# Optimization experiments

Measured on AMD Instinct MI355X. Metric: run time of the kernel, lower is better.

The kernel has to match this reference:

```python
import jax, jax.numpy as jnp
import numpy as np

LN_EPS = 1e-5

def _layernorm(x, gamma, beta):
    mu = jnp.mean(x, axis=-1, keepdims=True)
    var = jnp.mean((x - mu) ** 2, axis=-1, keepdims=True)
    return (x - mu) * jax.lax.rsqrt(var + LN_EPS) * gamma + beta

def setup_inputs() -> dict:
    key = jax.random.key(0)
    ks = jax.random.split(key, 12)
    n_drug, n_dis, E = 10000, 10000, 1000000
    feat = 128          # in_units * 2
    d_in = 2 * feat     # in_units * 4 = 256
    hid = 128
    hid2 = hid // 2
    def lin(kw, kb, fan_in, fan_out):
        bound = 1.0 / np.sqrt(fan_in)
        W = jax.random.uniform(kw, (fan_in, fan_out), jnp.float32, -bound, bound)
        b = jax.random.uniform(kb, (fan_out,), jnp.float32, -bound, bound)
        return W, b
    W1, b1 = lin(ks[0], ks[1], d_in, hid)
    W2, b2 = lin(ks[2], ks[3], hid, hid2)
    W3, b3 = lin(ks[4], ks[5], hid2, 1)
    return {
        "drug_feat": jax.random.normal(ks[6], (n_drug, feat), jnp.float32),
        "dis_feat": jax.random.normal(ks[7], (n_dis, feat), jnp.float32),
        "src_idx": jax.random.randint(ks[8], (E,), 0, n_drug, jnp.int32),
        "dst_idx": jax.random.randint(ks[9], (E,), 0, n_dis, jnp.int32),
        "W1": W1, "b1": b1,
        "g1": jnp.ones((hid,), jnp.float32), "be1": jnp.zeros((hid,), jnp.float32),
        "W2": W2, "b2": b2,
        "g2": jnp.ones((hid2,), jnp.float32), "be2": jnp.zeros((hid2,), jnp.float32),
        "W3": W3, "b3": b3,
    }

def reference(drug_feat, dis_feat, src_idx, dst_idx,
              W1, b1, g1, be1, W2, b2, g2, be2, W3, b3):
    # apply_edges: gather src (drug) and dst (disease) features, concat -> [E, 4*in_units]
    m = jnp.concatenate([drug_feat[src_idx], dis_feat[dst_idx]], axis=1)
    h = jax.nn.gelu(_layernorm(m @ W1 + b1, g1, be1), approximate=False)
    h = jax.nn.gelu(_layernorm(h @ W2 + b2, g2, be2), approximate=False)
    return h @ W3 + b3  # [E, 1]
```

## Files before the change

### kernel.cpp

```cpp
#include <hip/hip_runtime.h>
#include <hip/hip_bf16.h>

typedef __attribute__((ext_vector_type(4))) float f32x4;
typedef __attribute__((ext_vector_type(8))) short bf16x8;

#define MFMA16(a, b, c) __builtin_amdgcn_mfma_f32_16x16x32_bf16((a), (b), (c), 0, 0, 0)

#define W1T_OFF 0
#define B1_OFF  65536
#define G1_OFF  66048
#define E1_OFF  66560
#define B2_OFF  67072
#define G2_OFF  67328
#define E2_OFF  67584
#define W3_OFF  67840
#define B3_OFF  68096
#define SMEM_BYTES 68128

__device__ __forceinline__ short f2bf(float x) {
  __hip_bfloat16 h = __float2bfloat16(x);
  return __builtin_bit_cast(short, h);
}

__device__ __forceinline__ bf16x8 pack8(f32x4 a, f32x4 b) {
  bf16x8 r;
  r[0] = f2bf(a[0]); r[1] = f2bf(a[1]); r[2] = f2bf(a[2]); r[3] = f2bf(a[3]);
  r[4] = f2bf(b[0]); r[5] = f2bf(b[1]); r[6] = f2bf(b[2]); r[7] = f2bf(b[3]);
  return r;
}

__device__ __forceinline__ float gelu_fast(float z) {
  float s = z * z;
  float y = z * __builtin_fmaf(-0.10180479f, s, -2.3048496f);
  float t = __builtin_amdgcn_exp2f(y);
  return z * __builtin_amdgcn_rcpf(1.0f + t);
}

__global__ __launch_bounds__(256) void prep_weights(
    const float* __restrict__ W1, const float* __restrict__ W2,
    short* __restrict__ w1i, short* __restrict__ w2L) {
  int idx = blockIdx.x * 256 + threadIdx.x;
  if (idx < 32768) {
    int k = idx >> 7, n = idx & 127;
    w1i[n * 256 + ((((k >> 3) ^ (n & 7)) << 3) | (k & 7))] = f2bf(W1[idx]);
  } else if (idx < 40960) {
    int j = idx - 32768;
    int n = j >> 6, n2 = j & 63;
    int kb2 = n >> 5;
    int qf = (n >> 2) & 3;
    int e = ((n >> 4) & 1) * 4 + (n & 3);
    int t = n2 >> 4, cc2 = n2 & 15;
    w2L[(kb2 * 4 + t) * 512 + (qf * 16 + cc2) * 8 + e] = f2bf(W2[j]);
  }
}

__global__ __launch_bounds__(256) void prep_feats(
    const float* __restrict__ f, short* __restrict__ o, int n8) {
  int idx = blockIdx.x * 256 + threadIdx.x;
  if (idx < n8) {
    f32x4 a = *(const f32x4*)(f + idx * 8);
    f32x4 b = *(const f32x4*)(f + idx * 8 + 4);
    *(bf16x8*)(o + idx * 8) = pack8(a, b);
  }
}

__global__ __launch_bounds__(1024) __attribute__((amdgpu_waves_per_eu(2)))
void mlp_fused(
    const short* __restrict__ drugb, const short* __restrict__ disb,
    const int* __restrict__ src, const int* __restrict__ dst,
    const short* __restrict__ w1i, const short* __restrict__ w2L,
    const float* __restrict__ b1, const float* __restrict__ g1, const float* __restrict__ be1,
    const float* __restrict__ b2, const float* __restrict__ g2, const float* __restrict__ be2,
    const float* __restrict__ W3, const float* __restrict__ b3,
    float* __restrict__ out, int E, int ntiles) {
  extern __shared__ char smem[];
  short* w1t = (short*)(smem + W1T_OFF);
  float* b1s = (float*)(smem + B1_OFF);
  float* g1s = (float*)(smem + G1_OFF);
  float* e1s = (float*)(smem + E1_OFF);
  float* b2s = (float*)(smem + B2_OFF);
  float* g2s = (float*)(smem + G2_OFF);
  float* e2s = (float*)(smem + E2_OFF);
  float* w3s = (float*)(smem + W3_OFF);
  float* b3s = (float*)(smem + B3_OFF);

  const int tid  = threadIdx.x;
  const int wave = tid >> 6;
  const int lane = tid & 63;
  const int q    = lane >> 4;
  const int cc   = lane & 15;

  #pragma unroll
  for (int o = 0; o < 4; ++o) {
    int s = (tid + o * 1024) * 8;
    *(bf16x8*)(w1t + s) = *(const bf16x8*)(w1i + s);
  }
  if (tid < 128) { b1s[tid] = b1[tid]; g1s[tid] = g1[tid]; e1s[tid] = be1[tid]; }
  else if (tid < 192) { int j = tid - 128; b2s[j] = b2[j]; g2s[j] = g2[j]; e2s[j] = be2[j]; w3s[j] = W3[j]; }
  if (tid == 256) b3s[0] = b3[0];
  __syncthreads();

  const short* w2p = w2L + (lane << 3);

  for (int tile = blockIdx.x; tile < ntiles; tile += gridDim.x) {
    const int r  = tile * 256 + wave * 16 + cc;
    const int rc = (r < E) ? r : (E - 1);
    const short* pd = drugb + (size_t)src[rc] * 128 + q * 8;
    const short* pq = disb  + (size_t)dst[rc] * 128 + q * 8;

    f32x4 acc1[8];
    #pragma unroll
    for (int nt = 0; nt < 8; ++nt)
      acc1[nt] = *(const f32x4*)(b1s + nt * 16 + q * 4);

    bf16x8 u = *(const bf16x8*)pd;
    #pragma unroll 1
    for (int kb = 0; kb < 8; ++kb) {
      bf16x8 bfr = u;
      if (kb < 7) {
        const short* pn = (kb < 3) ? (pd + (kb + 1) * 32) : (pq + (kb - 3) * 32);
        u = *(const bf16x8*)pn;
      }
      const char* abase = (const char*)w1t + cc * 512 + ((((kb * 4 + q) ^ (cc & 7))) << 4);
      #pragma unroll
      for (int nt = 0; nt < 8; ++nt) {
        bf16x8 af = *(const bf16x8*)(abase + nt * 8192);
        acc1[nt] = MFMA16(af, bfr, acc1[nt]);
      }
    }

    bf16x8 hreg[4];
    {
      float s = 0.f, ss = 0.f;
      #pragma unroll
      for (int nt = 0; nt < 8; ++nt)
        #pragma unroll
        for (int j = 0; j < 4; ++j) { float v = acc1[nt][j]; s += v; ss += v * v; }
      s  += __shfl_xor(s, 16);  s  += __shfl_xor(s, 32);
      ss += __shfl_xor(ss, 16); ss += __shfl_xor(ss, 32);
      float mu   = s * 0.0078125f;
      float var  = ss * 0.0078125f - mu * mu;
      var = (var > 0.f) ? var : 0.f;
      float rstd = __builtin_amdgcn_rsqf(var + 1e-5f);

      #pragma unroll
      for (int h = 0; h < 4; ++h) {
        f32x4 glo = *(const f32x4*)(g1s + (2 * h) * 16 + q * 4);
        f32x4 elo = *(const f32x4*)(e1s + (2 * h) * 16 + q * 4);
        f32x4 ghi = *(const f32x4*)(g1s + (2 * h + 1) * 16 + q * 4);
        f32x4 ehi = *(const f32x4*)(e1s + (2 * h + 1) * 16 + q * 4);
        f32x4 a, b;
        #pragma unroll
        for (int j = 0; j < 4; ++j) {
          a[j] = gelu_fast(__builtin_fmaf((acc1[2 * h][j] - mu) * rstd, glo[j], elo[j]));
          b[j] = gelu_fast(__builtin_fmaf((acc1[2 * h + 1][j] - mu) * rstd, ghi[j], ehi[j]));
        }
        hreg[h] = pack8(a, b);
      }
    }

    f32x4 acc2[4];
    #pragma unroll
    for (int t = 0; t < 4; ++t)
      acc2[t] = *(const f32x4*)(b2s + t * 16 + q * 4);

    #pragma unroll
    for (int kb2 = 0; kb2 < 4; ++kb2) {
      bf16x8 hb = hreg[kb2];
      #pragma unroll
      for (int t = 0; t < 4; ++t) {
        bf16x8 af = *(const bf16x8*)(w2p + (kb2 * 4 + t) * 512);
        acc2[t] = MFMA16(af, hb, acc2[t]);
      }
      __builtin_amdgcn_sched_barrier(0);
    }

    {
      float s = 0.f, ss = 0.f;
      #pragma unroll
      for (int t = 0; t < 4; ++t)
        #pragma unroll
        for (int j = 0; j < 4; ++j) { float v = acc2[t][j]; s += v; ss += v * v; }
      s  += __shfl_xor(s, 16);  s  += __shfl_xor(s, 32);
      ss += __shfl_xor(ss, 16); ss += __shfl_xor(ss, 32);
      float mu   = s * 0.015625f;
      float var  = ss * 0.015625f - mu * mu;
      var = (var > 0.f) ? var : 0.f;
      float rstd = __builtin_amdgcn_rsqf(var + 1e-5f);

      float dot = 0.f;
      #pragma unroll
      for (int t = 0; t < 4; ++t) {
        f32x4 gv = *(const f32x4*)(g2s + t * 16 + q * 4);
        f32x4 ev = *(const f32x4*)(e2s + t * 16 + q * 4);
        f32x4 wv = *(const f32x4*)(w3s + t * 16 + q * 4);
        #pragma unroll
        for (int j = 0; j < 4; ++j) {
          float zz = __builtin_fmaf((acc2[t][j] - mu) * rstd, gv[j], ev[j]);
          dot = __builtin_fmaf(gelu_fast(zz), wv[j], dot);
        }
      }
      dot += __shfl_xor(dot, 16); dot += __shfl_xor(dot, 32);
      if (q == 0 && r < E) out[r] = dot + b3s[0];
    }
  }
}

extern "C" void kernel_launch(void* const* d_in, const int* in_sizes, int n_in,
                              void* d_out, int out_size, void* d_ws, size_t ws_size,
                              hipStream_t stream) {
  const float* drug = (const float*)d_in[0];
  const float* dis  = (const float*)d_in[1];
  const int*   src  = (const int*)d_in[2];
  const int*   dst  = (const int*)d_in[3];
  const float* W1   = (const float*)d_in[4];
  const float* b1   = (const float*)d_in[5];
  const float* g1   = (const float*)d_in[6];
  const float* be1  = (const float*)d_in[7];
  const float* W2   = (const float*)d_in[8];
  const float* b2   = (const float*)d_in[9];
  const float* g2   = (const float*)d_in[10];
  const float* be2  = (const float*)d_in[11];
  const float* W3   = (const float*)d_in[12];
  const float* b3   = (const float*)d_in[13];
  float* out = (float*)d_out;

  const int E      = in_sizes[2];
  const int ndrug8 = in_sizes[0] / 8;
  const int ndis8  = in_sizes[1] / 8;
  const int ntiles = (E + 255) / 256;

  short* w1i   = (short*)d_ws;
  short* w2L   = w1i + 32768;
  short* drugb = w2L + 8192;
  short* disb  = drugb + (size_t)ndrug8 * 8;

  (void)hipFuncSetAttribute((const void*)mlp_fused,
                            hipFuncAttributeMaxDynamicSharedMemorySize, SMEM_BYTES);

  prep_weights<<<dim3(160), dim3(256), 0, stream>>>(W1, W2, w1i, w2L);
  prep_feats<<<dim3((ndrug8 + 255) / 256), dim3(256), 0, stream>>>(drug, drugb, ndrug8);
  prep_feats<<<dim3((ndis8 + 255) / 256), dim3(256), 0, stream>>>(dis, disb, ndis8);

  int grid = 512;
  if (ntiles < grid) grid = ntiles;
  mlp_fused<<<dim3(grid), dim3(1024), SMEM_BYTES, stream>>>(
      drugb, disb, src, dst, w1i, w2L,
      b1, g1, be1, b2, g2, be2, W3, b3, out, E, ntiles);
}
```

Before: 247.5 us.

## Process two 16-row edge groups per wave to reuse W1/W2 LDS fragments

Each wave now handles 32 edges (two 16-row MFMA column blocks) instead of 16, so every W1 and W2 fragment read from LDS feeds two MFMAs. The block shrinks to 512 threads with launch bounds of 2 blocks per CU, keeping 256 edges per tile. This halves LDS traffic per edge and gives more independent MFMAs to hide latency. The cost is roughly double the accumulator registers per wave, which lowers occupancy and means fewer in-flight waves for gather latency.

```diff
diff --git a/kernel.cpp b/kernel.cpp
--- a/kernel.cpp
+++ b/kernel.cpp
@@ -64,8 +64,7 @@
   }
 }
 
-__global__ __launch_bounds__(1024) __attribute__((amdgpu_waves_per_eu(2)))
-void mlp_fused(
+__global__ __launch_bounds__(512, 2) void mlp_fused(
     const short* __restrict__ drugb, const short* __restrict__ disb,
     const int* __restrict__ src, const int* __restrict__ dst,
     const short* __restrict__ w1i, const short* __restrict__ w2L,
@@ -91,8 +90,8 @@
   const int cc   = lane & 15;
 
   #pragma unroll
-  for (int o = 0; o < 4; ++o) {
-    int s = (tid + o * 1024) * 8;
+  for (int o = 0; o < 8; ++o) {
+    int s = (tid + o * 512) * 8;
     *(bf16x8*)(w1t + s) = *(const bf16x8*)(w1i + s);
   }
   if (tid < 128) { b1s[tid] = b1[tid]; g1s[tid] = g1[tid]; e1s[tid] = be1[tid]; }
@@ -103,45 +102,63 @@
   const short* w2p = w2L + (lane << 3);
 
   for (int tile = blockIdx.x; tile < ntiles; tile += gridDim.x) {
-    const int r  = tile * 256 + wave * 16 + cc;
-    const int rc = (r < E) ? r : (E - 1);
-    const short* pd = drugb + (size_t)src[rc] * 128 + q * 8;
-    const short* pq = disb  + (size_t)dst[rc] * 128 + q * 8;
-
-    f32x4 acc1[8];
+    const int r0  = tile * 256 + wave * 32 + cc;
+    const int rc0 = (r0 < E) ? r0 : (E - 1);
+    const int rc1 = (r0 + 16 < E) ? (r0 + 16) : (E - 1);
+    const short* pd0 = drugb + (size_t)src[rc0] * 128 + q * 8;
+    const short* pq0 = disb  + (size_t)dst[rc0] * 128 + q * 8;
+    const short* pd1 = drugb + (size_t)src[rc1] * 128 + q * 8;
+    const short* pq1 = disb  + (size_t)dst[rc1] * 128 + q * 8;
+
+    f32x4 acc1[8][2];
     #pragma unroll
-    for (int nt = 0; nt < 8; ++nt)
-      acc1[nt] = *(const f32x4*)(b1s + nt * 16 + q * 4);
-
-    bf16x8 u = *(const bf16x8*)pd;
+    for (int nt = 0; nt < 8; ++nt) {
+      f32x4 bv = *(const f32x4*)(b1s + nt * 16 + q * 4);
+      acc1[nt][0] = bv;
+      acc1[nt][1] = bv;
+    }
+
+    bf16x8 u0 = *(const bf16x8*)pd0;
+    bf16x8 u1 = *(const bf16x8*)pd1;
     #pragma unroll 1
     for (int kb = 0; kb < 8; ++kb) {
-      bf16x8 bfr = u;
+      bf16x8 f0 = u0, f1 = u1;
       if (kb < 7) {
-        const short* pn = (kb < 3) ? (pd + (kb + 1) * 32) : (pq + (kb - 3) * 32);
-        u = *(const bf16x8*)pn;
+        const short* pn0 = (kb < 3) ? (pd0 + (kb + 1) * 32) : (pq0 + (kb - 3) * 32);
+        const short* pn1 = (kb < 3) ? (pd1 + (kb + 1) * 32) : (pq1 + (kb - 3) * 32);
+        u0 = *(const bf16x8*)pn0;
+        u1 = *(const bf16x8*)pn1;
       }
       const char* abase = (const char*)w1t + cc * 512 + ((((kb * 4 + q) ^ (cc & 7))) << 4);
       #pragma unroll
       for (int nt = 0; nt < 8; ++nt) {
         bf16x8 af = *(const bf16x8*)(abase + nt * 8192);
-        acc1[nt] = MFMA16(af, bfr, acc1[nt]);
-      }
-    }
-
-    bf16x8 hreg[4];
+        acc1[nt][0] = MFMA16(af, f0, acc1[nt][0]);
+        acc1[nt][1] = MFMA16(af, f1, acc1[nt][1]);
+      }
+    }
+
+    bf16x8 hreg[4][2];
     {
-      float s = 0.f, ss = 0.f;
+      float s0 = 0.f, ss0 = 0.f, s1 = 0.f, ss1 = 0.f;
       #pragma unroll
       for (int nt = 0; nt < 8; ++nt)
         #pragma unroll
-        for (int j = 0; j < 4; ++j) { float v = acc1[nt][j]; s += v; ss += v * v; }
-      s  += __shfl_xor(s, 16);  s  += __shfl_xor(s, 32);
-      ss += __shfl_xor(ss, 16); ss += __shfl_xor(ss, 32);
-      float mu   = s * 0.0078125f;
-      float var  = ss * 0.0078125f - mu * mu;
-      var = (var > 0.f) ? var : 0.f;
-      float rstd = __builtin_amdgcn_rsqf(var + 1e-5f);
+        for (int j = 0; j < 4; ++j) {
+          float v0 = acc1[nt][0][j]; s0 += v0; ss0 += v0 * v0;
+          float v1 = acc1[nt][1][j]; s1 += v1; ss1 += v1 * v1;
+        }
+      s0  += __shfl_xor(s0, 16);  s0  += __shfl_xor(s0, 32);
+      ss0 += __shfl_xor(ss0, 16); ss0 += __shfl_xor(ss0, 32);
+      s1  += __shfl_xor(s1, 16);  s1  += __shfl_xor(s1, 32);
+      ss1 += __shfl_xor(ss1, 16); ss1 += __shfl_xor(ss1, 32);
+      float mu0 = s0 * 0.0078125f, mu1 = s1 * 0.0078125f;
+      float va0 = ss0 * 0.0078125f - mu0 * mu0;
+      float va1 = ss1 * 0.0078125f - mu1 * mu1;
+      va0 = (va0 > 0.f) ? va0 : 0.f;
+      va1 = (va1 > 0.f) ? va1 : 0.f;
+      float rs0 = __builtin_amdgcn_rsqf(va0 + 1e-5f);
+      float rs1 = __builtin_amdgcn_rsqf(va1 + 1e-5f);
 
       #pragma unroll
       for (int h = 0; h < 4; ++h) {
@@ -149,46 +166,62 @@
         f32x4 elo = *(const f32x4*)(e1s + (2 * h) * 16 + q * 4);
         f32x4 ghi = *(const f32x4*)(g1s + (2 * h + 1) * 16 + q * 4);
         f32x4 ehi = *(const f32x4*)(e1s + (2 * h + 1) * 16 + q * 4);
-        f32x4 a, b;
-        #pragma unroll
-        for (int j = 0; j < 4; ++j) {
-          a[j] = gelu_fast(__builtin_fmaf((acc1[2 * h][j] - mu) * rstd, glo[j], elo[j]));
-          b[j] = gelu_fast(__builtin_fmaf((acc1[2 * h + 1][j] - mu) * rstd, ghi[j], ehi[j]));
-        }
-        hreg[h] = pack8(a, b);
-      }
-    }
-
-    f32x4 acc2[4];
+        f32x4 a0, b0, a1, b1v;
+        #pragma unroll
+        for (int j = 0; j < 4; ++j) {
+          a0[j]  = gelu_fast(__builtin_fmaf((acc1[2 * h][0][j]     - mu0) * rs0, glo[j], elo[j]));
+          b0[j]  = gelu_fast(__builtin_fmaf((acc1[2 * h + 1][0][j] - mu0) * rs0, ghi[j], ehi[j]));
+          a1[j]  = gelu_fast(__builtin_fmaf((acc1[2 * h][1][j]     - mu1) * rs1, glo[j], elo[j]));
+          b1v[j] = gelu_fast(__builtin_fmaf((acc1[2 * h + 1][1][j] - mu1) * rs1, ghi[j], ehi[j]));
+        }
+        hreg[h][0] = pack8(a0, b0);
+        hreg[h][1] = pack8(a1, b1v);
+      }
+    }
+
+    f32x4 acc2[4][2];
     #pragma unroll
-    for (int t = 0; t < 4; ++t)
-      acc2[t] = *(const f32x4*)(b2s + t * 16 + q * 4);
+    for (int t = 0; t < 4; ++t) {
+      f32x4 bv = *(const f32x4*)(b2s + t * 16 + q * 4);
+      acc2[t][0] = bv;
+      acc2[t][1] = bv;
+    }
 
     #pragma unroll
     for (int kb2 = 0; kb2 < 4; ++kb2) {
-      bf16x8 hb = hreg[kb2];
+      bf16x8 h0 = hreg[kb2][0];
+      bf16x8 h1 = hreg[kb2][1];
       #pragma unroll
       for (int t = 0; t < 4; ++t) {
         bf16x8 af = *(const bf16x8*)(w2p + (kb2 * 4 + t) * 512);
-        acc2[t] = MFMA16(af, hb, acc2[t]);
+        acc2[t][0] = MFMA16(af, h0, acc2[t][0]);
+        acc2[t][1] = MFMA16(af, h1, acc2[t][1]);
       }
       __builtin_amdgcn_sched_barrier(0);
     }
 
     {
-      float s = 0.f, ss = 0.f;
+      float s0 = 0.f, ss0 = 0.f, s1 = 0.f, ss1 = 0.f;
       #pragma unroll
       for (int t = 0; t < 4; ++t)
         #pragma unroll
-        for (int j = 0; j < 4; ++j) { float v = acc2[t][j]; s += v; ss += v * v; }
-      s  += __shfl_xor(s, 16);  s  += __shfl_xor(s, 32);
-      ss += __shfl_xor(ss, 16); ss += __shfl_xor(ss, 32);
-      float mu   = s * 0.015625f;
-      float var  = ss * 0.015625f - mu * mu;
-      var = (var > 0.f) ? var : 0.f;
-      float rstd = __builtin_amdgcn_rsqf(var + 1e-5f);
-
-      float dot = 0.f;
+        for (int j = 0; j < 4; ++j) {
+          float v0 = acc2[t][0][j]; s0 += v0; ss0 += v0 * v0;
+          float v1 = acc2[t][1][j]; s1 += v1; ss1 += v1 * v1;
+        }
+      s0  += __shfl_xor(s0, 16);  s0  += __shfl_xor(s0, 32);
+      ss0 += __shfl_xor(ss0, 16); ss0 += __shfl_xor(ss0, 32);
+      s1  += __shfl_xor(s1, 16);  s1  += __shfl_xor(s1, 32);
+      ss1 += __shfl_xor(ss1, 16); ss1 += __shfl_xor(ss1, 32);
+      float mu0 = s0 * 0.015625f, mu1 = s1 * 0.015625f;
+      float va0 = ss0 * 0.015625f - mu0 * mu0;
+      float va1 = ss1 * 0.015625f - mu1 * mu1;
+      va0 = (va0 > 0.f) ? va0 : 0.f;
+      va1 = (va1 > 0.f) ? va1 : 0.f;
+      float rs0 = __builtin_amdgcn_rsqf(va0 + 1e-5f);
+      float rs1 = __builtin_amdgcn_rsqf(va1 + 1e-5f);
+
+      float dot0 = 0.f, dot1 = 0.f;
       #pragma unroll
       for (int t = 0; t < 4; ++t) {
         f32x4 gv = *(const f32x4*)(g2s + t * 16 + q * 4);
@@ -196,12 +229,19 @@
         f32x4 wv = *(const f32x4*)(w3s + t * 16 + q * 4);
         #pragma unroll
         for (int j = 0; j < 4; ++j) {
-          float zz = __builtin_fmaf((acc2[t][j] - mu) * rstd, gv[j], ev[j]);
-          dot = __builtin_fmaf(gelu_fast(zz), wv[j], dot);
-        }
-      }
-      dot += __shfl_xor(dot, 16); dot += __shfl_xor(dot, 32);
-      if (q == 0 && r < E) out[r] = dot + b3s[0];
+          float z0 = __builtin_fmaf((acc2[t][0][j] - mu0) * rs0, gv[j], ev[j]);
+          float z1 = __builtin_fmaf((acc2[t][1][j] - mu1) * rs1, gv[j], ev[j]);
+          dot0 = __builtin_fmaf(gelu_fast(z0), wv[j], dot0);
+          dot1 = __builtin_fmaf(gelu_fast(z1), wv[j], dot1);
+        }
+      }
+      dot0 += __shfl_xor(dot0, 16); dot0 += __shfl_xor(dot0, 32);
+      dot1 += __shfl_xor(dot1, 16); dot1 += __shfl_xor(dot1, 32);
+      if (q == 0) {
+        float bias3 = b3s[0];
+        if (r0 < E)      out[r0]      = dot0 + bias3;
+        if (r0 + 16 < E) out[r0 + 16] = dot1 + bias3;
+      }
     }
   }
 }
@@ -244,7 +284,7 @@
 
   int grid = 512;
   if (ntiles < grid) grid = ntiles;
-  mlp_fused<<<dim3(grid), dim3(1024), SMEM_BYTES, stream>>>(
+  mlp_fused<<<dim3(grid), dim3(512), SMEM_BYTES, stream>>>(
       drugb, disb, src, dst, w1i, w2L,
       b1, g1, be1, b2, g2, be2, W3, b3, out, E, ntiles);
 }
```

Result: faster. 237.7 us (-4.0%).
